# Kernel optimization log

Measured on AMD Instinct MI355X. Metric: run time of the kernel, lower is better.

The kernel has to match this reference:

```python
import jax, jax.numpy as jnp
import numpy as np

LN_EPS = 1e-5   # torch LayerNorm default
NRM_EPS = 1e-8  # normalizer-state epsilon in mLSTMCell


def setup_inputs() -> dict:
    key = jax.random.key(0)
    ks = jax.random.split(key, 3)
    B, T, H, L, O = 32, 256, 1024, 4, 256
    x = jax.random.normal(ks[0], (B, T, H), dtype=jnp.float32)
    # 6 projections per layer in order (q, k, v, i, f, o); Linear stored as [in, out]
    W = jax.random.normal(ks[1], (L, 6, H, H), dtype=jnp.float32) * 0.02
    b = jnp.zeros((L, 6, H), dtype=jnp.float32)
    ln_g = jnp.ones((L, 6, H), dtype=jnp.float32)
    ln_b = jnp.zeros((L, 6, H), dtype=jnp.float32)
    fc_w = jax.random.normal(ks[2], (H, O), dtype=jnp.float32) * 0.02
    fc_b = jnp.zeros((O,), dtype=jnp.float32)
    return {"x": x, "W": W, "b": b, "ln_g": ln_g, "ln_b": ln_b,
            "fc_w": fc_w, "fc_b": fc_b}


def _layer_norm(z, g, beta):
    # z: [6, B, H]; g, beta: [6, H]
    mu = z.mean(-1, keepdims=True)
    var = z.var(-1, keepdims=True)
    return (z - mu) * jax.lax.rsqrt(var + LN_EPS) * g[:, None, :] + beta[:, None, :]


def _cell(x_in, h_prev, c_prev, n_prev, Wl, bl, gl, betal):
    # x_in: [B, H]; states: [B, H]; Wl: [6, H, H]
    z = jnp.einsum('bh,jhd->jbd', x_in, Wl) + bl[:, None, :]
    z = _layer_norm(z, gl, betal)
    q, k, v, zi, zf, zo = z  # q is computed by the original cell but unused
    i = jnp.exp(zi)
    f = jax.nn.sigmoid(zf)
    o = jax.nn.sigmoid(zo)
    # kv_interaction = outer(k, v); sum over dim=1 == sum(k) * v (same math, no [B,H,H])
    kv_sum = k.sum(-1, keepdims=True) * v
    c = f * c_prev + i * kv_sum
    n = f * n_prev + i * k
    n_hat = n / (jnp.linalg.norm(n, axis=-1, keepdims=True) + NRM_EPS)
    h = o * jnp.tanh(c * n_hat)
    return h, c, n


def _mlstm_forward(x, W, b, ln_g, ln_b, fc_w, fc_b):
    B, T, H = x.shape
    L = W.shape[0]
    h0 = jnp.zeros((L, B, H), x.dtype)
    init = (h0, h0, h0)  # (h, c, n)

    def step(carry, x_t):
        h, c, n = carry
        layer_in = x_t
        hs, cs, ns = [], [], []
        for l in range(L):  # small fixed layer count
            h_l, c_l, n_l = _cell(layer_in, h[l], c[l], n[l],
                                  W[l], b[l], ln_g[l], ln_b[l])
            if l > 0:  # residual connection (use_residual=True)
                h_l = h_l + layer_in
            layer_in = h_l
            hs.append(h_l); cs.append(c_l); ns.append(n_l)
        return (jnp.stack(hs), jnp.stack(cs), jnp.stack(ns)), None

    (h, c, n), _ = jax.lax.scan(step, init, jnp.swapaxes(x, 0, 1))
    # output[-1] == top-layer hidden at the final timestep
    out = h[-1] @ fc_w + fc_b  # [B, O]
    return out, (h, c, n)


def reference(x, W, b, ln_g, ln_b, fc_w, fc_b):
    return _mlstm_forward(x, W, b, ln_g, ln_b, fc_w, fc_b)
```

## Files before the change

kernel.cpp:

```cpp
#include <hip/hip_runtime.h>
#include <hip/hip_bf16.h>
#include <math.h>

#define H 1024
#define B 32
#define T 256
#define L 4
#define O 256
#define SEGLEN 16
#define NSEG (T / SEGLEN)

typedef _Float16 half8 __attribute__((ext_vector_type(8)));
typedef _Float16 half4 __attribute__((ext_vector_type(4)));
typedef float f32x4 __attribute__((ext_vector_type(4)));

#define X_PK_OFF   0
#define HB0_OFF    8388608
#define HB1_OFF    16777216
#define WT2_OFF    25165824
#define Z16_OFF    46137344
#define SEGA_OFF   88080384
#define SEGBC_OFF  89128960
#define SEGBN_OFF  90177536
#define STATS_OFF  91226112
#define CARC_OFF   91422720
#define CARN_OFF   92471296
#define FCP_OFF    93519872

__global__ __launch_bounds__(256) void pack_w(const float* __restrict__ W,
                                              _Float16* __restrict__ Wt2) {
  int tile = blockIdx.x;
  int m_idx = tile >> 8;
  int kt = (tile >> 4) & 15, ntt = tile & 15;
  int l = m_idx / 5, jj = m_idx % 5;
  const float* Wf = W + ((size_t)(l * 6 + jj + 1) << 20);
  _Float16* out = Wt2 + ((size_t)m_idx << 20);
  __shared__ float ts[64][65];
  int k0 = kt * 64, n0 = ntt * 64;
#pragma unroll
  for (int s = 0; s < 16; ++s) {
    int e = threadIdx.x + s * 256;
    int kk = e >> 6, col = e & 63;
    ts[kk][col] = Wf[(size_t)(k0 + kk) * H + n0 + col];
  }
  __syncthreads();
#pragma unroll
  for (int gi = 0; gi < 2; ++gi) {
    int g = threadIdx.x * 2 + gi;
    int l64 = g & 63, ksl = (g >> 6) & 1, ntl = g >> 7;
    int nn = l64 & 15, kh = l64 >> 4;
    half8 tmp;
#pragma unroll
    for (int e = 0; e < 8; ++e)
      tmp[e] = (_Float16)ts[ksl * 32 + kh * 8 + e][ntl * 16 + nn];
    *(half8*)&out[(size_t)((ntt * 4 + ntl) * 32 + kt * 2 + ksl) * 512 + (size_t)l64 * 8] = tmp;
  }
}

__global__ __launch_bounds__(256) void pack_x(const float* __restrict__ x,
                                              _Float16* __restrict__ x_pk) {
  int t = blockIdx.x;
  __shared__ float ld[32][257];
  for (int c = 0; c < 4; ++c) {
#pragma unroll
    for (int s = 0; s < 32; ++s) {
      int e2 = threadIdx.x + s * 256;
      int b = e2 >> 8, col = e2 & 255;
      ld[b][col] = x[((size_t)b * T + t) * H + c * 256 + col];
    }
    __syncthreads();
#pragma unroll
    for (int s3 = 0; s3 < 4; ++s3) {
      int gg = threadIdx.x * 4 + s3;
      int l64 = gg & 63, ksl = (gg >> 6) & 7, bt = gg >> 9;
      int nn = l64 & 15, kh = l64 >> 4;
      int b = bt * 16 + nn;
      half8 tmp;
#pragma unroll
      for (int e = 0; e < 8; ++e)
        tmp[e] = (_Float16)ld[b][ksl * 32 + kh * 8 + e];
      *(half8*)&x_pk[(size_t)t * 32768 + (size_t)bt * 16384 +
                     (size_t)(c * 8 + ksl) * 512 + (size_t)l64 * 8] = tmp;
    }
    __syncthreads();
  }
}

__global__ __launch_bounds__(512) void gemm_big(
    const _Float16* __restrict__ A_pk, const _Float16* __restrict__ Wl,
    _Float16* __restrict__ z16) {
  int raw = blockIdx.x;
  int xcd = raw & 7, c = raw >> 3;
  int bm = (xcd >> 1) * 16 + (c & 15);
  int bn = (xcd & 1) * 10 + (c >> 4);
  int w = threadIdx.x >> 6, lane = threadIdx.x & 63;
  int wm = w >> 2, wn = w & 3;

  __shared__ _Float16 smem[24576];

  int j = bn >> 2;
  const _Float16* gsrc[3];
  int ldst[3];
#pragma unroll
  for (int q = 0; q < 3; ++q) {
    int f = w * 3 + q;
    if (f < 8) {
      gsrc[q] = A_pk + (size_t)(bm * 8 + f) * 16384 + lane * 8;
      ldst[q] = f * 512 + lane * 8;
    } else {
      int nf = f - 8;
      gsrc[q] = Wl + ((size_t)j << 20) + (size_t)((bn & 3) * 16 + nf) * 16384 + lane * 8;
      ldst[q] = 4096 + nf * 512 + lane * 8;
    }
  }

  half8 stA[3], stB[3];
#pragma unroll
  for (int q = 0; q < 3; ++q) stA[q] = *(const half8*)(gsrc[q]);
#pragma unroll
  for (int q = 0; q < 3; ++q) *(half8*)&smem[ldst[q]] = stA[q];
#pragma unroll
  for (int q = 0; q < 3; ++q) stA[q] = *(const half8*)(gsrc[q] + 512);
  __syncthreads();

  f32x4 acc[4][4] = {};
  int ardo = wm * 2048 + lane * 8;
  int brdo = 4096 + wn * 2048 + lane * 8;

  for (int ks = 0; ks < 32; ks += 2) {
    {
      if (ks + 2 < 32) {
#pragma unroll
        for (int q = 0; q < 3; ++q)
          stB[q] = *(const half8*)(gsrc[q] + (size_t)(ks + 2) * 512);
      }
      half8 a[4], b[4];
#pragma unroll
      for (int i = 0; i < 4; ++i) a[i] = *(const half8*)&smem[ardo + i * 512];
#pragma unroll
      for (int i = 0; i < 4; ++i) b[i] = *(const half8*)&smem[brdo + i * 512];
#pragma unroll
      for (int i = 0; i < 4; ++i)
#pragma unroll
        for (int jf = 0; jf < 4; ++jf)
          acc[i][jf] = __builtin_amdgcn_mfma_f32_16x16x32_f16(a[i], b[jf], acc[i][jf], 0, 0, 0);
#pragma unroll
      for (int q = 0; q < 3; ++q) *(half8*)&smem[12288 + ldst[q]] = stA[q];
      asm volatile("s_waitcnt lgkmcnt(0)" ::: "memory");
      __builtin_amdgcn_s_barrier();
      __builtin_amdgcn_sched_barrier(0);
    }
    {
      if (ks + 3 < 32) {
#pragma unroll
        for (int q = 0; q < 3; ++q)
          stA[q] = *(const half8*)(gsrc[q] + (size_t)(ks + 3) * 512);
      }
      half8 a[4], b[4];
#pragma unroll
      for (int i = 0; i < 4; ++i) a[i] = *(const half8*)&smem[12288 + ardo + i * 512];
#pragma unroll
      for (int i = 0; i < 4; ++i) b[i] = *(const half8*)&smem[12288 + brdo + i * 512];
#pragma unroll
      for (int i = 0; i < 4; ++i)
#pragma unroll
        for (int jf = 0; jf < 4; ++jf)
          acc[i][jf] = __builtin_amdgcn_mfma_f32_16x16x32_f16(a[i], b[jf], acc[i][jf], 0, 0, 0);
      if (ks + 2 < 32) {
#pragma unroll
        for (int q = 0; q < 3; ++q) *(half8*)&smem[ldst[q]] = stB[q];
        asm volatile("s_waitcnt lgkmcnt(0)" ::: "memory");
        __builtin_amdgcn_s_barrier();
        __builtin_amdgcn_sched_barrier(0);
      }
    }
  }
  __syncthreads();

  _Float16 (*cz)[264] = (_Float16(*)[264])smem;
  int hb0 = (bn & 3) * 256;
  for (int p = 0; p < 2; ++p) {
    if (p) __syncthreads();
    if (wm == p) {
#pragma unroll
      for (int i = 0; i < 4; ++i)
#pragma unroll
        for (int jf = 0; jf < 4; ++jf)
#pragma unroll
          for (int r = 0; r < 4; ++r)
            cz[i * 16 + (lane >> 4) * 4 + r][wn * 64 + jf * 16 + (lane & 15)] =
                (_Float16)acc[i][jf][r];
    }
    __syncthreads();
#pragma unroll
    for (int s = 0; s < 4; ++s) {
      int e = threadIdx.x + s * 512;
      int r = e >> 5, h8 = e & 31;
      int m_local = bm * 128 + p * 64 + r;
      half8 vv = *(const half8*)&cz[r][h8 * 8];
      *(half8*)&z16[((size_t)m_local * 5 + j) * 1024 + hb0 + h8 * 8] = vv;
    }
  }
}

__global__ __launch_bounds__(256) void scan_p1fused(
    const _Float16* __restrict__ z16, const float* __restrict__ bias,
    const float* __restrict__ ln_g, const float* __restrict__ ln_b,
    float* __restrict__ stats, float* __restrict__ segA,
    float* __restrict__ segBc, float* __restrict__ segBn, int l) {
  int seg = blockIdx.x >> 5, b = blockIdx.x & 31;
  int tid = threadIdx.x, h0 = tid * 4;

  float bz[5][4], gg[5][4], bb[5][4];
#pragma unroll
  for (int jj = 0; jj < 5; ++jj) {
    float4 t1 = *(const float4*)&bias[(size_t)(l * 6 + 1 + jj) * H + h0];
    float4 t2 = *(const float4*)&ln_g[(size_t)(l * 6 + 1 + jj) * H + h0];
    float4 t3 = *(const float4*)&ln_b[(size_t)(l * 6 + 1 + jj) * H + h0];
    bz[jj][0] = t1.x; bz[jj][1] = t1.y; bz[jj][2] = t1.z; bz[jj][3] = t1.w;
    gg[jj][0] = t2.x; gg[jj][1] = t2.y; gg[jj][2] = t2.z; gg[jj][3] = t2.w;
    bb[jj][0] = t3.x; bb[jj][1] = t3.y; bb[jj][2] = t3.z; bb[jj][3] = t3.w;
  }

  float A[4] = {1.f, 1.f, 1.f, 1.f};
  float bc[4] = {0.f, 0.f, 0.f, 0.f};
  float bn[4] = {0.f, 0.f, 0.f, 0.f};
  __shared__ float sb[4][13];

  half4 zr[5];
  {
    int row0 = (seg * SEGLEN) * 32 + b;
#pragma unroll
    for (int jj = 0; jj < 5; ++jj)
      zr[jj] = *(const half4*)&z16[((size_t)row0 * 5 + jj) * 1024 + h0];
  }

  for (int u = 0; u < SEGLEN; ++u) {
    int row = (seg * SEGLEN + u) * 32 + b;
    half4 zc[5];
#pragma unroll
    for (int jj = 0; jj < 5; ++jj) zc[jj] = zr[jj];
    if (u + 1 < SEGLEN) {
      int rown = (seg * SEGLEN + u + 1) * 32 + b;
#pragma unroll
      for (int jj = 0; jj < 5; ++jj)
        zr[jj] = *(const half4*)&z16[((size_t)rown * 5 + jj) * 1024 + h0];
    }
    float v[5][4];
    float red[13];
#pragma unroll
    for (int jj = 0; jj < 5; ++jj) {
      float s = 0.f, sq = 0.f;
#pragma unroll
      for (int e = 0; e < 4; ++e) {
        float val = (float)zc[jj][e] + bz[jj][e];
        v[jj][e] = val;
        s += val;
        sq += val * val;
      }
      red[jj * 2] = s;
      red[jj * 2 + 1] = sq;
      if (jj == 0) {
        red[10] = v[0][0] * gg[0][0] + v[0][1] * gg[0][1] +
                  v[0][2] * gg[0][2] + v[0][3] * gg[0][3];
        red[11] = gg[0][0] + gg[0][1] + gg[0][2] + gg[0][3];
        red[12] = bb[0][0] + bb[0][1] + bb[0][2] + bb[0][3];
      }
    }
#pragma unroll
    for (int off = 32; off; off >>= 1)
#pragma unroll
      for (int q = 0; q < 13; ++q) red[q] += __shfl_xor(red[q], off);
    if ((tid & 63) == 0) {
#pragma unroll
      for (int q = 0; q < 13; ++q) sb[tid >> 6][q] = red[q];
    }
    __syncthreads();
    float st[13];
#pragma unroll
    for (int q = 0; q < 13; ++q)
      st[q] = sb[0][q] + sb[1][q] + sb[2][q] + sb[3][q];
    __syncthreads();

    float mus[5], rss[5];
#pragma unroll
    for (int jj = 0; jj < 5; ++jj) {
      float mu = st[jj * 2] * (1.0f / H);
      float var = st[jj * 2 + 1] * (1.0f / H) - mu * mu;
      mus[jj] = mu;
      rss[jj] = rsqrtf(var + 1e-5f);
    }
    float ksum = rss[0] * (st[10] - mus[0] * st[11]) + st[12];
    if (tid < 12) {
      float val;
      if (tid < 10) val = (tid & 1) ? rss[tid >> 1] : mus[tid >> 1];
      else if (tid == 10) val = ksum;
      else val = 0.f;
      stats[(size_t)row * 12 + tid] = val;
    }
#pragma unroll
    for (int e = 0; e < 4; ++e) {
      float k   = (v[0][e] - mus[0]) * rss[0] * gg[0][e] + bb[0][e];
      float vv  = (v[1][e] - mus[1]) * rss[1] * gg[1][e] + bb[1][e];
      float zi_ = (v[2][e] - mus[2]) * rss[2] * gg[2][e] + bb[2][e];
      float zf_ = (v[3][e] - mus[3]) * rss[3] * gg[3][e] + bb[3][e];
      float iv = __expf(zi_);
      float fv = 1.f / (1.f + __expf(-zf_));
      A[e] *= fv;
      bn[e] = fv * bn[e] + iv * k;
      bc[e] = fv * bc[e] + iv * (ksum * vv);
    }
  }
  size_t so = ((size_t)seg * 32 + b) * 1024 + h0;
  *(float4*)&segA[so]  = make_float4(A[0], A[1], A[2], A[3]);
  *(float4*)&segBn[so] = make_float4(bn[0], bn[1], bn[2], bn[3]);
  *(float4*)&segBc[so] = make_float4(bc[0], bc[1], bc[2], bc[3]);
}

__global__ __launch_bounds__(256) void scan_p2(
    const float* __restrict__ segA, const float* __restrict__ segBc,
    const float* __restrict__ segBn, float* __restrict__ carC,
    float* __restrict__ carN) {
  int idx = blockIdx.x * 256 + threadIdx.x;
  int h = idx & 1023, b = idx >> 10;
  float cc = 0.f, nn = 0.f;
#pragma unroll
  for (int seg = 0; seg < NSEG; ++seg) {
    size_t coff = (size_t)seg * 32768 + (size_t)b * 1024 + h;
    carC[coff] = cc;
    carN[coff] = nn;
    size_t so = ((size_t)seg * 32 + b) * 1024 + h;
    float a = segA[so];
    cc = segBc[so] + a * cc;
    nn = segBn[so] + a * nn;
  }
}

__global__ __launch_bounds__(256) void final_scan(
    const _Float16* __restrict__ z16, const float* __restrict__ stats,
    const float* __restrict__ bias, const float* __restrict__ ln_g,
    const float* __restrict__ ln_b, const float* __restrict__ carC,
    const float* __restrict__ carN, const _Float16* __restrict__ hin,
    _Float16* __restrict__ hout, float* __restrict__ out, int l) {
  int seg = blockIdx.x >> 5, b = blockIdx.x & 31;
  int tid = threadIdx.x, h0 = tid * 4;

  float bz[5][4], gg[5][4], bb[5][4];
#pragma unroll
  for (int jj = 0; jj < 5; ++jj) {
    float4 t1 = *(const float4*)&bias[(size_t)(l * 6 + 1 + jj) * H + h0];
    float4 t2 = *(const float4*)&ln_g[(size_t)(l * 6 + 1 + jj) * H + h0];
    float4 t3 = *(const float4*)&ln_b[(size_t)(l * 6 + 1 + jj) * H + h0];
    bz[jj][0] = t1.x; bz[jj][1] = t1.y; bz[jj][2] = t1.z; bz[jj][3] = t1.w;
    gg[jj][0] = t2.x; gg[jj][1] = t2.y; gg[jj][2] = t2.z; gg[jj][3] = t2.w;
    bb[jj][0] = t3.x; bb[jj][1] = t3.y; bb[jj][2] = t3.z; bb[jj][3] = t3.w;
  }

  size_t coff = (size_t)seg * 32768 + (size_t)b * 1024 + h0;
  float4 cC4 = *(const float4*)&carC[coff];
  float4 cN4 = *(const float4*)&carN[coff];
  float c_[4] = {cC4.x, cC4.y, cC4.z, cC4.w};
  float n_[4] = {cN4.x, cN4.y, cN4.z, cN4.w};

  size_t hfoff = (size_t)(b >> 4) * 16384 + (size_t)(h0 >> 5) * 512 +
                 (size_t)((((h0 & 31) >> 3) * 16) + (b & 15)) * 8 + (h0 & 7);
  __shared__ float sbuf[2][4];

  half4 zr[5];
  {
    int row0 = (seg * SEGLEN) * 32 + b;
#pragma unroll
    for (int jj = 0; jj < 5; ++jj)
      zr[jj] = *(const half4*)&z16[((size_t)row0 * 5 + jj) * 1024 + h0];
  }

  for (int u = 0; u < SEGLEN; ++u) {
    int t = seg * SEGLEN + u;
    int row = t * 32 + b;
    half4 zc[5];
#pragma unroll
    for (int jj = 0; jj < 5; ++jj) zc[jj] = zr[jj];
    if (u + 1 < SEGLEN) {
      int rown = (t + 1) * 32 + b;
#pragma unroll
      for (int jj = 0; jj < 5; ++jj)
        zr[jj] = *(const half4*)&z16[((size_t)rown * 5 + jj) * 1024 + h0];
    }
    half4 rin;
    if (l > 0) rin = *(const half4*)&hin[(size_t)t * 32768 + hfoff];

    const float* st = stats + (size_t)row * 12;
    float mu0 = st[0], rs0 = st[1], mu1 = st[2], rs1 = st[3];
    float mu2 = st[4], rs2 = st[5], mu3 = st[6], rs3 = st[7];
    float mu4 = st[8], rs4 = st[9], ksum = st[10];

    float ss = 0.f;
#pragma unroll
    for (int e = 0; e < 4; ++e) {
      float k   = ((float)zc[0][e] + bz[0][e] - mu0) * rs0 * gg[0][e] + bb[0][e];
      float v   = ((float)zc[1][e] + bz[1][e] - mu1) * rs1 * gg[1][e] + bb[1][e];
      float zi_ = ((float)zc[2][e] + bz[2][e] - mu2) * rs2 * gg[2][e] + bb[2][e];
      float zf_ = ((float)zc[3][e] + bz[3][e] - mu3) * rs3 * gg[3][e] + bb[3][e];
      float iv = __expf(zi_);
      float fv = 1.f / (1.f + __expf(-zf_));
      n_[e] = fv * n_[e] + iv * k;
      c_[e] = fv * c_[e] + iv * (ksum * v);
      ss += n_[e] * n_[e];
    }
#pragma unroll
    for (int off = 32; off; off >>= 1) ss += __shfl_down(ss, off);
    if ((tid & 63) == 0) sbuf[u & 1][tid >> 6] = ss;
    __syncthreads();
    float nrm = sbuf[u & 1][0] + sbuf[u & 1][1] + sbuf[u & 1][2] + sbuf[u & 1][3];
    float rn = 1.f / (sqrtf(nrm) + 1e-8f);

    float hh[4];
#pragma unroll
    for (int e = 0; e < 4; ++e) {
      float zo_ = ((float)zc[4][e] + bz[4][e] - mu4) * rs4 * gg[4][e] + bb[4][e];
      float ov = 1.f / (1.f + __expf(-zo_));
      float targ = c_[e] * (n_[e] * rn);
      float e2 = __expf(-2.f * fabsf(targ));
      float th = copysignf((1.f - e2) / (1.f + e2), targ);
      hh[e] = ov * th + ((l > 0) ? (float)rin[e] : 0.f);
    }
    half4 hx;
    hx[0] = (_Float16)hh[0]; hx[1] = (_Float16)hh[1];
    hx[2] = (_Float16)hh[2]; hx[3] = (_Float16)hh[3];
    *(half4*)&hout[(size_t)t * 32768 + hfoff] = hx;

    if (t == T - 1) {
      *(float4*)&out[8192 + (size_t)l * 32768 + (size_t)b * 1024 + h0] =
          make_float4(hh[0], hh[1], hh[2], hh[3]);
      *(float4*)&out[8192 + 131072 + ((size_t)(l * B) + b) * 1024 + h0] =
          make_float4(c_[0], c_[1], c_[2], c_[3]);
      *(float4*)&out[8192 + 262144 + ((size_t)(l * B) + b) * 1024 + h0] =
          make_float4(n_[0], n_[1], n_[2], n_[3]);
    }
  }
}

__global__ __launch_bounds__(256) void fc_part(
    const float* __restrict__ out_h, const float* __restrict__ fc_w,
    float* __restrict__ partial) {
  int b = blockIdx.x >> 3, kh = blockIdx.x & 7;
  int o = threadIdx.x;
  const float* hr = out_h + (size_t)b * 1024 + kh * 128;
  const float* wp = fc_w + (size_t)kh * 128 * O + o;
  float acc = 0.f;
#pragma unroll 8
  for (int h = 0; h < 128; ++h)
    acc = fmaf(hr[h], wp[(size_t)h * O], acc);
  partial[((size_t)kh * 32 + b) * O + o] = acc;
}

__global__ __launch_bounds__(256) void fc_reduce(
    const float* __restrict__ partial, const float* __restrict__ fc_b,
    float* __restrict__ out) {
  int b = blockIdx.x, o = threadIdx.x;
  float acc = fc_b[o];
#pragma unroll
  for (int kh = 0; kh < 8; ++kh)
    acc += partial[((size_t)kh * 32 + b) * O + o];
  out[(size_t)b * O + o] = acc;
}

extern "C" void kernel_launch(void* const* d_in, const int* in_sizes, int n_in,
                              void* d_out, int out_size, void* d_ws, size_t ws_size,
                              hipStream_t stream) {
  const float* x    = (const float*)d_in[0];
  const float* W    = (const float*)d_in[1];
  const float* bias = (const float*)d_in[2];
  const float* ln_g = (const float*)d_in[3];
  const float* ln_b = (const float*)d_in[4];
  const float* fc_w = (const float*)d_in[5];
  const float* fc_b = (const float*)d_in[6];
  float* out = (float*)d_out;
  _Float16* wsh = (_Float16*)d_ws;

  _Float16* x_pk = wsh + X_PK_OFF;
  _Float16* hb[2] = {wsh + HB0_OFF, wsh + HB1_OFF};
  _Float16* Wt2  = wsh + WT2_OFF;
  _Float16* z16  = wsh + Z16_OFF;
  float* segA  = (float*)(wsh + SEGA_OFF);
  float* segBc = (float*)(wsh + SEGBC_OFF);
  float* segBn = (float*)(wsh + SEGBN_OFF);
  float* stats = (float*)(wsh + STATS_OFF);
  float* carC  = (float*)(wsh + CARC_OFF);
  float* carN  = (float*)(wsh + CARN_OFF);
  float* fcp   = (float*)(wsh + FCP_OFF);

  pack_w<<<5120, 256, 0, stream>>>(W, Wt2);
  pack_x<<<256, 256, 0, stream>>>(x, x_pk);

  for (int l = 0; l < L; ++l) {
    const _Float16* A_in = (l == 0) ? x_pk : hb[(l - 1) & 1];
    _Float16* h_out = hb[l & 1];
    const _Float16* Wl = Wt2 + ((size_t)(l * 5) << 20);
    gemm_big<<<1280, 512, 0, stream>>>(A_in, Wl, z16);
    scan_p1fused<<<512, 256, 0, stream>>>(z16, bias, ln_g, ln_b, stats,
                                          segA, segBc, segBn, l);
    scan_p2<<<128, 256, 0, stream>>>(segA, segBc, segBn, carC, carN);
    final_scan<<<512, 256, 0, stream>>>(z16, stats, bias, ln_g, ln_b,
                                        carC, carN, A_in, h_out, out, l);
  }
  fc_part<<<256, 256, 0, stream>>>(out + 8192 + 3 * 32768, fc_w, fcp);
  fc_reduce<<<B, 256, 0, stream>>>(fcp, fc_b, out);
}
```

Measured before the change: 767.1 us.

## Merge pack kernels, fold segment carry scan into final_scan, single-kernel FC

Combines the weight and input packing kernels into one launch, removes the separate scan_p2 carry kernel by having each final_scan block recompute its prefix carry from the segment summaries, and replaces the two-kernel split-K FC with one kernel per batch row. The aim is to cut kernel launches and drop the carry round trip through global memory. The cost is redundant prefix work in later segments, up to 15 serial steps, and a less parallel FC with 32 blocks each looping over 1024 inputs.

```diff
diff --git a/kernel.cpp b/kernel.cpp
--- a/kernel.cpp
+++ b/kernel.cpp
@@ -23,66 +23,65 @@
 #define SEGBC_OFF  89128960
 #define SEGBN_OFF  90177536
 #define STATS_OFF  91226112
-#define CARC_OFF   91422720
-#define CARN_OFF   92471296
-#define FCP_OFF    93519872
-
-__global__ __launch_bounds__(256) void pack_w(const float* __restrict__ W,
-                                              _Float16* __restrict__ Wt2) {
-  int tile = blockIdx.x;
-  int m_idx = tile >> 8;
-  int kt = (tile >> 4) & 15, ntt = tile & 15;
-  int l = m_idx / 5, jj = m_idx % 5;
-  const float* Wf = W + ((size_t)(l * 6 + jj + 1) << 20);
-  _Float16* out = Wt2 + ((size_t)m_idx << 20);
-  __shared__ float ts[64][65];
-  int k0 = kt * 64, n0 = ntt * 64;
-#pragma unroll
-  for (int s = 0; s < 16; ++s) {
-    int e = threadIdx.x + s * 256;
-    int kk = e >> 6, col = e & 63;
-    ts[kk][col] = Wf[(size_t)(k0 + kk) * H + n0 + col];
-  }
-  __syncthreads();
-#pragma unroll
-  for (int gi = 0; gi < 2; ++gi) {
-    int g = threadIdx.x * 2 + gi;
-    int l64 = g & 63, ksl = (g >> 6) & 1, ntl = g >> 7;
-    int nn = l64 & 15, kh = l64 >> 4;
-    half8 tmp;
-#pragma unroll
-    for (int e = 0; e < 8; ++e)
-      tmp[e] = (_Float16)ts[ksl * 32 + kh * 8 + e][ntl * 16 + nn];
-    *(half8*)&out[(size_t)((ntt * 4 + ntl) * 32 + kt * 2 + ksl) * 512 + (size_t)l64 * 8] = tmp;
-  }
-}
-
-__global__ __launch_bounds__(256) void pack_x(const float* __restrict__ x,
-                                              _Float16* __restrict__ x_pk) {
-  int t = blockIdx.x;
-  __shared__ float ld[32][257];
-  for (int c = 0; c < 4; ++c) {
-#pragma unroll
-    for (int s = 0; s < 32; ++s) {
-      int e2 = threadIdx.x + s * 256;
-      int b = e2 >> 8, col = e2 & 255;
-      ld[b][col] = x[((size_t)b * T + t) * H + c * 256 + col];
+
+__global__ __launch_bounds__(256) void pack_wx(
+    const float* __restrict__ W, const float* __restrict__ x,
+    _Float16* __restrict__ Wt2, _Float16* __restrict__ x_pk) {
+  __shared__ float shmem[32 * 257];
+  if (blockIdx.x < 5120) {
+    int tile = blockIdx.x;
+    int m_idx = tile >> 8;
+    int kt = (tile >> 4) & 15, ntt = tile & 15;
+    int l = m_idx / 5, jj = m_idx % 5;
+    const float* Wf = W + ((size_t)(l * 6 + jj + 1) << 20);
+    _Float16* out = Wt2 + ((size_t)m_idx << 20);
+    float (*ts)[65] = (float(*)[65])shmem;
+    int k0 = kt * 64, n0 = ntt * 64;
+#pragma unroll
+    for (int s = 0; s < 16; ++s) {
+      int e = threadIdx.x + s * 256;
+      int kk = e >> 6, col = e & 63;
+      ts[kk][col] = Wf[(size_t)(k0 + kk) * H + n0 + col];
     }
     __syncthreads();
 #pragma unroll
-    for (int s3 = 0; s3 < 4; ++s3) {
-      int gg = threadIdx.x * 4 + s3;
-      int l64 = gg & 63, ksl = (gg >> 6) & 7, bt = gg >> 9;
+    for (int gi = 0; gi < 2; ++gi) {
+      int g = threadIdx.x * 2 + gi;
+      int l64 = g & 63, ksl = (g >> 6) & 1, ntl = g >> 7;
       int nn = l64 & 15, kh = l64 >> 4;
-      int b = bt * 16 + nn;
       half8 tmp;
 #pragma unroll
       for (int e = 0; e < 8; ++e)
-        tmp[e] = (_Float16)ld[b][ksl * 32 + kh * 8 + e];
-      *(half8*)&x_pk[(size_t)t * 32768 + (size_t)bt * 16384 +
-                     (size_t)(c * 8 + ksl) * 512 + (size_t)l64 * 8] = tmp;
-    }
-    __syncthreads();
+        tmp[e] = (_Float16)ts[ksl * 32 + kh * 8 + e][ntl * 16 + nn];
+      *(half8*)&out[(size_t)((ntt * 4 + ntl) * 32 + kt * 2 + ksl) * 512 +
+                    (size_t)l64 * 8] = tmp;
+    }
+  } else {
+    int t = blockIdx.x - 5120;
+    float (*ld)[257] = (float(*)[257])shmem;
+    for (int c = 0; c < 4; ++c) {
+      if (c) __syncthreads();
+#pragma unroll
+      for (int s = 0; s < 32; ++s) {
+        int e2 = threadIdx.x + s * 256;
+        int b = e2 >> 8, col = e2 & 255;
+        ld[b][col] = x[((size_t)b * T + t) * H + c * 256 + col];
+      }
+      __syncthreads();
+#pragma unroll
+      for (int s3 = 0; s3 < 4; ++s3) {
+        int gg = threadIdx.x * 4 + s3;
+        int l64 = gg & 63, ksl = (gg >> 6) & 7, bt = gg >> 9;
+        int nn = l64 & 15, kh = l64 >> 4;
+        int b = bt * 16 + nn;
+        half8 tmp;
+#pragma unroll
+        for (int e = 0; e < 8; ++e)
+          tmp[e] = (_Float16)ld[b][ksl * 32 + kh * 8 + e];
+        *(half8*)&x_pk[(size_t)t * 32768 + (size_t)bt * 16384 +
+                       (size_t)(c * 8 + ksl) * 512 + (size_t)l64 * 8] = tmp;
+      }
+    }
   }
 }
 
@@ -317,31 +316,13 @@
   *(float4*)&segBc[so] = make_float4(bc[0], bc[1], bc[2], bc[3]);
 }
 
-__global__ __launch_bounds__(256) void scan_p2(
-    const float* __restrict__ segA, const float* __restrict__ segBc,
-    const float* __restrict__ segBn, float* __restrict__ carC,
-    float* __restrict__ carN) {
-  int idx = blockIdx.x * 256 + threadIdx.x;
-  int h = idx & 1023, b = idx >> 10;
-  float cc = 0.f, nn = 0.f;
-#pragma unroll
-  for (int seg = 0; seg < NSEG; ++seg) {
-    size_t coff = (size_t)seg * 32768 + (size_t)b * 1024 + h;
-    carC[coff] = cc;
-    carN[coff] = nn;
-    size_t so = ((size_t)seg * 32 + b) * 1024 + h;
-    float a = segA[so];
-    cc = segBc[so] + a * cc;
-    nn = segBn[so] + a * nn;
-  }
-}
-
 __global__ __launch_bounds__(256) void final_scan(
     const _Float16* __restrict__ z16, const float* __restrict__ stats,
     const float* __restrict__ bias, const float* __restrict__ ln_g,
-    const float* __restrict__ ln_b, const float* __restrict__ carC,
-    const float* __restrict__ carN, const _Float16* __restrict__ hin,
-    _Float16* __restrict__ hout, float* __restrict__ out, int l) {
+    const float* __restrict__ ln_b, const float* __restrict__ segA,
+    const float* __restrict__ segBc, const float* __restrict__ segBn,
+    const _Float16* __restrict__ hin, _Float16* __restrict__ hout,
+    float* __restrict__ out, int l) {
   int seg = blockIdx.x >> 5, b = blockIdx.x & 31;
   int tid = threadIdx.x, h0 = tid * 4;
 
@@ -356,11 +337,17 @@
     bb[jj][0] = t3.x; bb[jj][1] = t3.y; bb[jj][2] = t3.z; bb[jj][3] = t3.w;
   }
 
-  size_t coff = (size_t)seg * 32768 + (size_t)b * 1024 + h0;
-  float4 cC4 = *(const float4*)&carC[coff];
-  float4 cN4 = *(const float4*)&carN[coff];
-  float c_[4] = {cC4.x, cC4.y, cC4.z, cC4.w};
-  float n_[4] = {cN4.x, cN4.y, cN4.z, cN4.w};
+  float c_[4] = {0.f, 0.f, 0.f, 0.f}, n_[4] = {0.f, 0.f, 0.f, 0.f};
+  for (int s = 0; s < seg; ++s) {
+    size_t so = ((size_t)s * 32 + b) * 1024 + h0;
+    float4 a4  = *(const float4*)&segA[so];
+    float4 bc4 = *(const float4*)&segBc[so];
+    float4 bn4 = *(const float4*)&segBn[so];
+    c_[0] = bc4.x + a4.x * c_[0]; c_[1] = bc4.y + a4.y * c_[1];
+    c_[2] = bc4.z + a4.z * c_[2]; c_[3] = bc4.w + a4.w * c_[3];
+    n_[0] = bn4.x + a4.x * n_[0]; n_[1] = bn4.y + a4.y * n_[1];
+    n_[2] = bn4.z + a4.z * n_[2]; n_[3] = bn4.w + a4.w * n_[3];
+  }
 
   size_t hfoff = (size_t)(b >> 4) * 16384 + (size_t)(h0 >> 5) * 512 +
                  (size_t)((((h0 & 31) >> 3) * 16) + (b & 15)) * 8 + (h0 & 7);
@@ -440,28 +427,18 @@
   }
 }
 
-__global__ __launch_bounds__(256) void fc_part(
+__global__ __launch_bounds__(256) void fc_one(
     const float* __restrict__ out_h, const float* __restrict__ fc_w,
-    float* __restrict__ partial) {
-  int b = blockIdx.x >> 3, kh = blockIdx.x & 7;
+    const float* __restrict__ fc_b, float* __restrict__ out) {
+  int b = blockIdx.x;
   int o = threadIdx.x;
-  const float* hr = out_h + (size_t)b * 1024 + kh * 128;
-  const float* wp = fc_w + (size_t)kh * 128 * O + o;
-  float acc = 0.f;
+  __shared__ float hs[1024];
+  *(float4*)&hs[o * 4] = *(const float4*)&out_h[(size_t)b * 1024 + o * 4];
+  __syncthreads();
+  float acc = fc_b[o];
 #pragma unroll 8
-  for (int h = 0; h < 128; ++h)
-    acc = fmaf(hr[h], wp[(size_t)h * O], acc);
-  partial[((size_t)kh * 32 + b) * O + o] = acc;
-}
-
-__global__ __launch_bounds__(256) void fc_reduce(
-    const float* __restrict__ partial, const float* __restrict__ fc_b,
-    float* __restrict__ out) {
-  int b = blockIdx.x, o = threadIdx.x;
-  float acc = fc_b[o];
-#pragma unroll
-  for (int kh = 0; kh < 8; ++kh)
-    acc += partial[((size_t)kh * 32 + b) * O + o];
+  for (int h = 0; h < H; ++h)
+    acc = fmaf(hs[h], fc_w[(size_t)h * O + o], acc);
   out[(size_t)b * O + o] = acc;
 }
 
@@ -486,12 +463,8 @@
   float* segBc = (float*)(wsh + SEGBC_OFF);
   float* segBn = (float*)(wsh + SEGBN_OFF);
   float* stats = (float*)(wsh + STATS_OFF);
-  float* carC  = (float*)(wsh + CARC_OFF);
-  float* carN  = (float*)(wsh + CARN_OFF);
-  float* fcp   = (float*)(wsh + FCP_OFF);
-
-  pack_w<<<5120, 256, 0, stream>>>(W, Wt2);
-  pack_x<<<256, 256, 0, stream>>>(x, x_pk);
+
+  pack_wx<<<5376, 256, 0, stream>>>(W, x, Wt2, x_pk);
 
   for (int l = 0; l < L; ++l) {
     const _Float16* A_in = (l == 0) ? x_pk : hb[(l - 1) & 1];
@@ -500,10 +473,9 @@
     gemm_big<<<1280, 512, 0, stream>>>(A_in, Wl, z16);
     scan_p1fused<<<512, 256, 0, stream>>>(z16, bias, ln_g, ln_b, stats,
                                           segA, segBc, segBn, l);
-    scan_p2<<<128, 256, 0, stream>>>(segA, segBc, segBn, carC, carN);
     final_scan<<<512, 256, 0, stream>>>(z16, stats, bias, ln_g, ln_b,
-                                        carC, carN, A_in, h_out, out, l);
-  }
-  fc_part<<<256, 256, 0, stream>>>(out + 8192 + 3 * 32768, fc_w, fcp);
-  fc_reduce<<<B, 256, 0, stream>>>(fcp, fc_b, out);
-}
+                                        segA, segBc, segBn,
+                                        A_in, h_out, out, l);
+  }
+  fc_one<<<B, 256, 0, stream>>>(out + 8192 + 3 * 32768, fc_w, fc_b, out);
+}
```

After: 780.4 us. About the same (+1.7%).
